# Kernel tuning notes

Hardware: AMD Instinct MI355X
Metric: run time of the kernel (lower is better)

Reference implementation:

```python
import jax, jax.numpy as jnp
import numpy as np

B, LAT, H, F, L, NL = 128, 128, 512, 128, 256, 2


def setup_inputs() -> dict:
    key = jax.random.key(0)
    ks = jax.random.split(key, 20)
    s = 0.05  # keep recurrence well-conditioned
    def n(k, shp):
        return jax.random.normal(k, shp, dtype=jnp.float32) * s
    return dict(
        z=jax.random.normal(ks[0], (B, LAT), dtype=jnp.float32),
        W_l2h=n(ks[1], (H * NL, LAT)), b_l2h=n(ks[2], (H * NL,)),
        W_l2c=n(ks[3], (H * NL, LAT)), b_l2c=n(ks[4], (H * NL,)),
        W_zp=n(ks[5], (H, LAT)), b_zp=n(ks[6], (H,)),
        W_ih0=n(ks[7], (4 * H, F + H)), W_hh0=n(ks[8], (4 * H, H)),
        b_ih0=n(ks[9], (4 * H,)), b_hh0=n(ks[10], (4 * H,)),
        W_ih1=n(ks[11], (4 * H, H)), W_hh1=n(ks[12], (4 * H, H)),
        b_ih1=n(ks[13], (4 * H,)), b_hh1=n(ks[14], (4 * H,)),
        ln_g=jnp.ones((H,), jnp.float32), ln_b=jnp.zeros((H,), jnp.float32),
        W_pre=n(ks[15], (H, H)), b_pre=n(ks[16], (H,)),
        W_out=n(ks[17], (F, H)), b_out=n(ks[18], (F,)),
    )


def _lstm_cell(x, h, c, Wih, Whh, bih, bhh):
    # PyTorch gate order: i, f, g, o
    gates = x @ Wih.T + bih + h @ Whh.T + bhh
    i, f, g, o = jnp.split(gates, 4, axis=-1)
    c = jax.nn.sigmoid(f) * c + jax.nn.sigmoid(i) * jnp.tanh(g)
    h = jax.nn.sigmoid(o) * jnp.tanh(c)
    return h, c


def _layernorm(x, g, b, eps=1e-5):
    m = jnp.mean(x, axis=-1, keepdims=True)
    v = jnp.var(x, axis=-1, keepdims=True)
    return (x - m) * jax.lax.rsqrt(v + eps) * g + b


def reference(z, W_l2h, b_l2h, W_l2c, b_l2c, W_zp, b_zp,
              W_ih0, W_hh0, b_ih0, b_hh0, W_ih1, W_hh1, b_ih1, b_hh1,
              ln_g, ln_b, W_pre, b_pre, W_out, b_out):
    # Faithful to torch: (B, NL*H) viewed row-major as (NL, B, H)
    h0 = (z @ W_l2h.T + b_l2h).reshape(NL, B, H)
    c0 = (z @ W_l2c.T + b_l2c).reshape(NL, B, H)
    z_proj = z @ W_zp.T + b_zp  # (B, H), injected every step
    dec0 = jnp.zeros((B, F), dtype=z.dtype)

    def step(carry, _):
        ha, ca, hb, cb, dec = carry
        x = jnp.concatenate([dec, z_proj], axis=-1)  # (B, F+H)
        ha, ca = _lstm_cell(x, ha, ca, W_ih0, W_hh0, b_ih0, b_hh0)
        hb, cb = _lstm_cell(ha, hb, cb, W_ih1, W_hh1, b_ih1, b_hh1)
        ln = _layernorm(hb, ln_g, ln_b)
        pre = jax.nn.relu(ln @ W_pre.T + b_pre)
        out_t = (pre + ln) @ W_out.T + b_out  # residual through MLP
        return (ha, ca, hb, cb, out_t), out_t

    _, ys = jax.lax.scan(step, (h0[0], c0[0], h0[1], c0[1], dec0), None, length=L)
    return jnp.transpose(ys, (1, 0, 2))  # (B, L, F)
```

## Files before the change

kernel.cpp:

```cpp
#include <hip/hip_runtime.h>
#include <hip/hip_cooperative_groups.h>

namespace cg = cooperative_groups;


typedef unsigned int uint32;
typedef unsigned short u16;
typedef __attribute__((ext_vector_type(8))) short bf16x8;
typedef __attribute__((ext_vector_type(4))) float f32x4;

static constexpr int Ln = 256, Fn = 128;
static constexpr int APS = 65536;
static constexpr int WPS = 2097152;
static constexpr int OPS = 65536;
static constexpr int PPS = 262144;

static constexpr int BAR_REL = 4096;
static constexpr int BAR_WORDS = 4160;

static constexpr int ROWP = 520;
static constexpr int PLANE = 16 * ROWP;
static constexpr int SACT_ELEMS = 6 * PLANE;

static constexpr int SM_HV   = 0;
static constexpr int SM_LNH  = 33024;
static constexpr int SM_LNM  = 49664;
static constexpr int SM_LNL  = 66304;
static constexpr int SM_RED  = 82944;
static constexpr int SM_MEAN = 83968;
static constexpr int SM_RSTD = 84032;
static constexpr int SMEM_BYTES = 84096;

__device__ __forceinline__ u16 f2bf(float f) {
  union { float f; uint32 u; } v; v.f = f;
  uint32 u = v.u + 0x7fffu + ((v.u >> 16) & 1u);
  return (u16)(u >> 16);
}
__device__ __forceinline__ float bf2f(u16 h) {
  union { uint32 u; float f; } v; v.u = ((uint32)h) << 16;
  return v.f;
}
__device__ __forceinline__ void splitbf3(float v, u16* hi, u16* mid, u16* lo) {
  u16 h = f2bf(v);
  float r = v - bf2f(h);
  u16 m = f2bf(r);
  float r2 = r - bf2f(m);
  *hi = h; *mid = m; *lo = f2bf(r2);
}
__device__ __forceinline__ float sigm(float x) { return 1.f / (1.f + expf(-x)); }
__device__ __forceinline__ bf16x8 ldf(const u16* p) { return *(const bf16x8*)p; }

__device__ __forceinline__ bf16x8 ldc16(const u16* p) {
  bf16x8 r;
  asm volatile("global_load_dwordx4 %0, %1, off sc0 sc1" : "=v"(r) : "v"(p) : "memory");
  return r;
}
__device__ __forceinline__ void stc2(u16* p, u16 v) {
  asm volatile("global_store_short %0, %1, off sc0 sc1" :: "v"(p), "v"((uint32)v) : "memory");
}
__device__ __forceinline__ void vwait0_fence() {
  asm volatile("s_waitcnt vmcnt(0)" ::: "memory");
  __builtin_amdgcn_sched_barrier(0);
}

__device__ __forceinline__ void gbar(uint32* arr, uint32* rel, uint32 ep, int blk) {
  asm volatile("s_waitcnt vmcnt(0) lgkmcnt(0)" ::: "memory");
  __syncthreads();
  int tid = threadIdx.x;
  if (blk == 0) {
    for (;;) {
      uint32 v = __hip_atomic_load(&arr[tid * 16], __ATOMIC_RELAXED, __HIP_MEMORY_SCOPE_AGENT);
      if (__syncthreads_and((tid == 0) || (v >= ep))) break;
      __builtin_amdgcn_s_sleep(1);
    }
    if (tid == 0)
      __hip_atomic_store(rel, ep, __ATOMIC_RELAXED, __HIP_MEMORY_SCOPE_AGENT);
  } else {
    if (tid == 0) {
      __hip_atomic_store(&arr[blk * 16], ep, __ATOMIC_RELAXED, __HIP_MEMORY_SCOPE_AGENT);
      while (__hip_atomic_load(rel, __ATOMIC_RELAXED, __HIP_MEMORY_SCOPE_AGENT) < ep)
        __builtin_amdgcn_s_sleep(1);
    }
  }
  __syncthreads();
  __builtin_amdgcn_sched_barrier(0);
}

#define MFMA1(A, B, ACC) ACC = __builtin_amdgcn_mfma_f32_16x16x32_bf16((A), (B), (ACC), 0, 0, 0)
#define MFMA6(AH, AM, AL, BH, BM, BL, A0, A1, A2) \
  do {                                            \
    MFMA1(AH, BH, A0);                            \
    MFMA1(AH, BM, A1); MFMA1(AM, BH, A1);         \
    MFMA1(AH, BL, A2); MFMA1(AL, BH, A2);         \
    MFMA1(AM, BM, A2);                            \
  } while (0)


__device__ __forceinline__ void stage_side(const u16* __restrict__ g, int b0,
                                           u16* sAct, int sideBase, int tid) {
  bf16x8 tv[12];
#pragma unroll
  for (int jr = 0; jr < 12; ++jr) {
    int plane = jr >> 2;
    int c2 = tid + ((jr & 3) << 8);
    int row = c2 >> 6, col = c2 & 63;
    tv[jr] = ldc16(g + (size_t)plane * APS + (size_t)(b0 + row) * 512 + col * 8);
  }
  vwait0_fence();
#pragma unroll
  for (int jr = 0; jr < 12; ++jr) {
    int plane = jr >> 2;
    int c2 = tid + ((jr & 3) << 8);
    int row = c2 >> 6, col = c2 & 63;
    *(bf16x8*)&sAct[sideBase + plane * PLANE + row * ROWP + col * 8] = tv[jr];
  }
}

__device__ __forceinline__ void gate_tile_p(
    const u16* __restrict__ g0, const u16* __restrict__ g1,
    const u16* __restrict__ wr,
    const float* __restrict__ bias, int bias_stride,
    float& cr, u16* __restrict__ hout,
    int b0, int h0, int tid, u16* sAct, float (*gbuf)[16][16]) {
  stage_side(g0, b0, sAct, 0, tid);
  stage_side(g1, b0, sAct, 3 * PLANE, tid);
  __syncthreads();
  int lane = tid & 63, w = tid >> 6, q = lane >> 4, r16 = lane & 15;
  const u16* aB = sAct + r16 * ROWP + q * 8;
  f32x4 A0 = {0.f, 0.f, 0.f, 0.f}, A1 = {0.f, 0.f, 0.f, 0.f}, A2 = {0.f, 0.f, 0.f, 0.f};
#pragma unroll
  for (int kb = 0; kb < 16; ++kb) {
    bf16x8 ah = ldf(aB + kb * 32), am = ldf(aB + PLANE + kb * 32), al = ldf(aB + 2 * PLANE + kb * 32);
    bf16x8 bh = ldf(wr + kb * 32), bm = ldf(wr + WPS + kb * 32), bl = ldf(wr + 2 * WPS + kb * 32);
    MFMA6(ah, am, al, bh, bm, bl, A0, A1, A2);
  }
#pragma unroll
  for (int kb = 0; kb < 16; ++kb) {
    bf16x8 ah = ldf(aB + 3 * PLANE + kb * 32), am = ldf(aB + 4 * PLANE + kb * 32),
           al = ldf(aB + 5 * PLANE + kb * 32);
    bf16x8 bh = ldf(wr + 512 + kb * 32), bm = ldf(wr + WPS + 512 + kb * 32),
           bl = ldf(wr + 2 * WPS + 512 + kb * 32);
    MFMA6(ah, am, al, bh, bm, bl, A0, A1, A2);
  }
#pragma unroll
  for (int r = 0; r < 4; ++r)
    gbuf[w][q * 4 + r][r16] = (A2[r] + A1[r]) + A0[r];
  __syncthreads();
  int bl_ = tid >> 4, hl = tid & 15;
  int b = b0 + bl_, h = h0 + hl;
  const float* bb = bias + (size_t)b * bias_stride;
  float gi = gbuf[0][bl_][hl] + bb[h];
  float gf = gbuf[1][bl_][hl] + bb[512 + h];
  float gc = gbuf[2][bl_][hl] + bb[1024 + h];
  float go = gbuf[3][bl_][hl] + bb[1536 + h];
  int idx = b * 512 + h;
  float cn = sigm(gf) * cr + sigm(gi) * tanhf(gc);
  cr = cn;
  float hv_ = sigm(go) * tanhf(cn);
  u16 hh, hm, hl2;
  splitbf3(hv_, &hh, &hm, &hl2);
  stc2(hout + idx, hh);
  stc2(hout + APS + idx, hm);
  stc2(hout + 2 * APS + idx, hl2);
}

__device__ __forceinline__ void ys_tile_p(
    const u16* __restrict__ sg, const u16* __restrict__ wr,
    const float* __restrict__ b_out, float* __restrict__ ys,
    int tout, int b0, int f0, int tid, u16* sAct) {
  stage_side(sg, b0, sAct, 0, tid);
  __syncthreads();
  int lane = tid & 63, q = lane >> 4, r16 = lane & 15;
  const u16* aB = sAct + r16 * ROWP + q * 8;
  f32x4 A0 = {0.f, 0.f, 0.f, 0.f}, A1 = {0.f, 0.f, 0.f, 0.f}, A2 = {0.f, 0.f, 0.f, 0.f};
#pragma unroll
  for (int kb = 0; kb < 16; ++kb) {
    bf16x8 ah = ldf(aB + kb * 32), am = ldf(aB + PLANE + kb * 32), al = ldf(aB + 2 * PLANE + kb * 32);
    bf16x8 bh = ldf(wr + kb * 32), bm = ldf(wr + OPS + kb * 32), bl = ldf(wr + 2 * OPS + kb * 32);
    MFMA6(ah, am, al, bh, bm, bl, A0, A1, A2);
  }
  int fc = f0 + r16;
  float bo = b_out[fc];
#pragma unroll
  for (int r = 0; r < 4; ++r) {
    int b = b0 + q * 4 + r;
    ys[(size_t)b * (Ln * Fn) + (size_t)tout * Fn + fc] = ((A2[r] + A1[r]) + A0[r]) + bo;
  }
}

__device__ __forceinline__ void lnpre_tile_p(
    const u16* __restrict__ hb, const u16* __restrict__ wr,
    const float* __restrict__ lng, const float* __restrict__ lnb,
    const float* __restrict__ b_pre, u16* __restrict__ s_out,
    int j0, int b0, int tid, char* smem) {
  float* hv = (float*)(smem + SM_HV);
  u16* lnH = (u16*)(smem + SM_LNH);
  u16* lnM = (u16*)(smem + SM_LNM);
  u16* lnL = (u16*)(smem + SM_LNL);
  float (*red)[16] = (float (*)[16])(smem + SM_RED);
  float* smean = (float*)(smem + SM_MEAN);
  float* srstd = (float*)(smem + SM_RSTD);
  bf16x8 p[12];
#pragma unroll
  for (int jj = 0; jj < 4; ++jj) {
    int c = tid + 256 * jj;
    int b = c >> 6, k0 = (c & 63) * 8;
    size_t base = (size_t)(b0 + b) * 512 + k0;
    p[jj * 3 + 0] = ldc16(hb + base);
    p[jj * 3 + 1] = ldc16(hb + APS + base);
    p[jj * 3 + 2] = ldc16(hb + 2 * APS + base);
  }
  vwait0_fence();
#pragma unroll
  for (int jj = 0; jj < 4; ++jj) {
    int c = tid + 256 * jj;
    int b = c >> 6, k0 = (c & 63) * 8;
#pragma unroll
    for (int e = 0; e < 8; ++e)
      hv[b * 516 + k0 + e] = (bf2f((u16)p[jj * 3 + 2][e]) + bf2f((u16)p[jj * 3 + 1][e])) +
                             bf2f((u16)p[jj * 3 + 0][e]);
  }
  __syncthreads();
  int bl_ = tid >> 4, kc = tid & 15;
  {
    float sm = 0.f;
    for (int kk = 0; kk < 32; ++kk) sm += hv[bl_ * 516 + kc * 32 + kk];
    red[bl_][kc] = sm;
  }
  __syncthreads();
  if (tid < 16) {
    float s1 = 0.f;
    for (int i = 0; i < 16; ++i) s1 += red[tid][i];
    smean[tid] = s1 * (1.f / 512.f);
  }
  __syncthreads();
  {
    float m = smean[bl_], sq = 0.f;
    for (int kk = 0; kk < 32; ++kk) {
      float d = hv[bl_ * 516 + kc * 32 + kk] - m;
      sq += d * d;
    }
    red[bl_][kc] = sq;
  }
  __syncthreads();
  if (tid < 16) {
    float s2 = 0.f;
    for (int i = 0; i < 16; ++i) s2 += red[tid][i];
    srstd[tid] = 1.f / sqrtf(s2 * (1.f / 512.f) + 1e-5f);
  }
  __syncthreads();
  for (int i = tid; i < 16 * 512; i += 256) {
    int b = i >> 9, k = i & 511;
    float v = (hv[b * 516 + k] - smean[b]) * srstd[b] * lng[k] + lnb[k];
    splitbf3(v, &lnH[b * 520 + k], &lnM[b * 520 + k], &lnL[b * 520 + k]);
  }
  __syncthreads();
  int lane = tid & 63, w = tid >> 6, q = lane >> 4, r16 = lane & 15;
  const u16* aH = lnH + r16 * 520 + q * 8;
  const u16* aM = lnM + r16 * 520 + q * 8;
  const u16* aL = lnL + r16 * 520 + q * 8;
  f32x4 A0 = {0.f, 0.f, 0.f, 0.f}, A1 = {0.f, 0.f, 0.f, 0.f}, A2 = {0.f, 0.f, 0.f, 0.f};
#pragma unroll
  for (int kb = 0; kb < 16; ++kb) {
    bf16x8 ah = ldf(aH + kb * 32), am = ldf(aM + kb * 32), al = ldf(aL + kb * 32);
    bf16x8 bh = ldf(wr + kb * 32), bm = ldf(wr + PPS + kb * 32), bl = ldf(wr + 2 * PPS + kb * 32);
    MFMA6(ah, am, al, bh, bm, bl, A0, A1, A2);
  }
  int j = j0 + w * 16 + r16;
  float bp = b_pre[j];
#pragma unroll
  for (int r = 0; r < 4; ++r) {
    int b = q * 4 + r;
    float lnv = (hv[b * 516 + j] - smean[b]) * srstd[b] * lng[j] + lnb[j];
    float pre = fmaxf(((A2[r] + A1[r]) + A0[r]) + bp, 0.f);
    float sval = pre + lnv;
    size_t sidx = (size_t)(b0 + b) * 512 + j;
    u16 sh, sm_, sl;
    splitbf3(sval, &sh, &sm_, &sl);
    stc2(s_out + sidx, sh);
    stc2(s_out + APS + sidx, sm_);
    stc2(s_out + 2 * APS + sidx, sl);
  }
}


__device__ __forceinline__ void gate_tile(
    const u16* __restrict__ a0, const u16* __restrict__ a1,
    const u16* __restrict__ wr,
    const float* __restrict__ bias, int bias_stride,
    float* __restrict__ cstate, u16* __restrict__ hout,
    int b0, int h0, int tid, float (*gbuf)[16][16]) {
  int w = tid >> 6;
  int lane = tid & 63, q = lane >> 4, r16 = lane & 15;
  f32x4 A0 = {0.f, 0.f, 0.f, 0.f}, A1 = {0.f, 0.f, 0.f, 0.f}, A2 = {0.f, 0.f, 0.f, 0.f};
#pragma unroll
  for (int kb = 0; kb < 16; ++kb) {
    bf16x8 ah = ldf(a0 + kb * 32), am = ldf(a0 + APS + kb * 32), al = ldf(a0 + 2 * APS + kb * 32);
    bf16x8 bh = ldf(wr + kb * 32), bm = ldf(wr + WPS + kb * 32), bl = ldf(wr + 2 * WPS + kb * 32);
    MFMA6(ah, am, al, bh, bm, bl, A0, A1, A2);
  }
#pragma unroll
  for (int kb = 0; kb < 16; ++kb) {
    bf16x8 ah = ldf(a1 + kb * 32), am = ldf(a1 + APS + kb * 32), al = ldf(a1 + 2 * APS + kb * 32);
    bf16x8 bh = ldf(wr + 512 + kb * 32), bm = ldf(wr + WPS + 512 + kb * 32),
           bl = ldf(wr + 2 * WPS + 512 + kb * 32);
    MFMA6(ah, am, al, bh, bm, bl, A0, A1, A2);
  }
#pragma unroll
  for (int r = 0; r < 4; ++r)
    gbuf[w][q * 4 + r][r16] = (A2[r] + A1[r]) + A0[r];
  __syncthreads();
  int bl_ = tid >> 4, hl = tid & 15;
  int b = b0 + bl_, h = h0 + hl;
  const float* bb = bias + (size_t)b * bias_stride;
  float gi = gbuf[0][bl_][hl] + bb[h];
  float gf = gbuf[1][bl_][hl] + bb[512 + h];
  float gc = gbuf[2][bl_][hl] + bb[1024 + h];
  float go = gbuf[3][bl_][hl] + bb[1536 + h];
  int idx = b * 512 + h;
  float c = cstate[idx];
  float cn = sigm(gf) * c + sigm(gi) * tanhf(gc);
  cstate[idx] = cn;
  float hv_ = sigm(go) * tanhf(cn);
  splitbf3(hv_, &hout[idx], &hout[APS + idx], &hout[2 * APS + idx]);
  __syncthreads();
}

__device__ __forceinline__ void ys_tile(
    const u16* __restrict__ a, const u16* __restrict__ wr,
    const float* __restrict__ b_out, float* __restrict__ ys,
    int tout, int b0, int f0, int tid) {
  int lane = tid & 63, q = lane >> 4, r16 = lane & 15;
  f32x4 A0 = {0.f, 0.f, 0.f, 0.f}, A1 = {0.f, 0.f, 0.f, 0.f}, A2 = {0.f, 0.f, 0.f, 0.f};
#pragma unroll
  for (int kb = 0; kb < 16; ++kb) {
    bf16x8 ah = ldf(a + kb * 32), am = ldf(a + APS + kb * 32), al = ldf(a + 2 * APS + kb * 32);
    bf16x8 bh = ldf(wr + kb * 32), bm = ldf(wr + OPS + kb * 32), bl = ldf(wr + 2 * OPS + kb * 32);
    MFMA6(ah, am, al, bh, bm, bl, A0, A1, A2);
  }
  int fc = f0 + r16;
  float bo = b_out[fc];
#pragma unroll
  for (int r = 0; r < 4; ++r) {
    int b = b0 + q * 4 + r;
    ys[(size_t)b * (Ln * Fn) + (size_t)tout * Fn + fc] = ((A2[r] + A1[r]) + A0[r]) + bo;
  }
}

__device__ __forceinline__ void lnpre_tile(
    const u16* __restrict__ hb, const u16* __restrict__ wr,
    const float* __restrict__ lng, const float* __restrict__ lnb,
    const float* __restrict__ b_pre, u16* __restrict__ s_out,
    int j0, int b0, int tid, char* smem) {
  float* hv = (float*)(smem + SM_HV);
  u16* lnH = (u16*)(smem + SM_LNH);
  u16* lnM = (u16*)(smem + SM_LNM);
  u16* lnL = (u16*)(smem + SM_LNL);
  float (*red)[16] = (float (*)[16])(smem + SM_RED);
  float* smean = (float*)(smem + SM_MEAN);
  float* srstd = (float*)(smem + SM_RSTD);
  for (int i = tid; i < 16 * 512; i += 256) {
    int b = i >> 9, k = i & 511;
    size_t hidx = (size_t)(b0 + b) * 512 + k;
    hv[b * 516 + k] = (bf2f(hb[2 * APS + hidx]) + bf2f(hb[APS + hidx])) + bf2f(hb[hidx]);
  }
  __syncthreads();
  int bl_ = tid >> 4, kc = tid & 15;
  {
    float sm = 0.f;
    for (int kk = 0; kk < 32; ++kk) sm += hv[bl_ * 516 + kc * 32 + kk];
    red[bl_][kc] = sm;
  }
  __syncthreads();
  if (tid < 16) {
    float s1 = 0.f;
    for (int i = 0; i < 16; ++i) s1 += red[tid][i];
    smean[tid] = s1 * (1.f / 512.f);
  }
  __syncthreads();
  {
    float m = smean[bl_], sq = 0.f;
    for (int kk = 0; kk < 32; ++kk) {
      float d = hv[bl_ * 516 + kc * 32 + kk] - m;
      sq += d * d;
    }
    red[bl_][kc] = sq;
  }
  __syncthreads();
  if (tid < 16) {
    float s2 = 0.f;
    for (int i = 0; i < 16; ++i) s2 += red[tid][i];
    srstd[tid] = 1.f / sqrtf(s2 * (1.f / 512.f) + 1e-5f);
  }
  __syncthreads();
  for (int i = tid; i < 16 * 512; i += 256) {
    int b = i >> 9, k = i & 511;
    float v = (hv[b * 516 + k] - smean[b]) * srstd[b] * lng[k] + lnb[k];
    splitbf3(v, &lnH[b * 520 + k], &lnM[b * 520 + k], &lnL[b * 520 + k]);
  }
  __syncthreads();
  int lane = tid & 63, w = tid >> 6, q = lane >> 4, r16 = lane & 15;
  const u16* aH = lnH + r16 * 520 + q * 8;
  const u16* aM = lnM + r16 * 520 + q * 8;
  const u16* aL = lnL + r16 * 520 + q * 8;
  f32x4 A0 = {0.f, 0.f, 0.f, 0.f}, A1 = {0.f, 0.f, 0.f, 0.f}, A2 = {0.f, 0.f, 0.f, 0.f};
#pragma unroll
  for (int kb = 0; kb < 16; ++kb) {
    bf16x8 ah = ldf(aH + kb * 32), am = ldf(aM + kb * 32), al = ldf(aL + kb * 32);
    bf16x8 bh = ldf(wr + kb * 32), bm = ldf(wr + PPS + kb * 32), bl = ldf(wr + 2 * PPS + kb * 32);
    MFMA6(ah, am, al, bh, bm, bl, A0, A1, A2);
  }
  int j = j0 + w * 16 + r16;
  float bp = b_pre[j];
#pragma unroll
  for (int r = 0; r < 4; ++r) {
    int b = q * 4 + r;
    float lnv = (hv[b * 516 + j] - smean[b]) * srstd[b] * lng[j] + lnb[j];
    float pre = fmaxf(((A2[r] + A1[r]) + A0[r]) + bp, 0.f);
    float sval = pre + lnv;
    size_t sidx = (size_t)(b0 + b) * 512 + j;
    splitbf3(sval, &s_out[sidx], &s_out[APS + sidx], &s_out[2 * APS + sidx]);
  }
  __syncthreads();
}


__global__ void prep_hc0(const float* __restrict__ z,
                         const float* __restrict__ W_l2h, const float* __restrict__ b_l2h,
                         const float* __restrict__ W_l2c, const float* __restrict__ b_l2c,
                         u16* __restrict__ ha0, u16* __restrict__ hb0,
                         float* __restrict__ ca, float* __restrict__ cb) {
  int idx = blockIdx.x * 256 + threadIdx.x;
  int b = idx & 127, j = idx >> 7;
  float ah = b_l2h[j], ac = b_l2c[j];
  for (int k = 0; k < 128; ++k) {
    float zv = z[b * 128 + k];
    ah += zv * W_l2h[j * 128 + k];
    ac += zv * W_l2c[j * 128 + k];
  }
  int flat = b * 1024 + j;
  if (flat < 65536) {
    splitbf3(ah, &ha0[flat], &ha0[APS + flat], &ha0[2 * APS + flat]);
    ca[flat] = ac;
  } else {
    flat -= 65536;
    splitbf3(ah, &hb0[flat], &hb0[APS + flat], &hb0[2 * APS + flat]);
    cb[flat] = ac;
  }
}

__global__ void prep_zp(const float* __restrict__ z, const float* __restrict__ W_zp,
                        const float* __restrict__ b_zp, float* __restrict__ zp) {
  int idx = blockIdx.x * 256 + threadIdx.x;
  int b = idx & 127, h = idx >> 7;
  float a = b_zp[h];
  for (int k = 0; k < 128; ++k) a += z[b * 128 + k] * W_zp[h * 128 + k];
  zp[b * 512 + h] = a;
}

__global__ void prep_gz(const float* __restrict__ zp, const float* __restrict__ W_ih0,
                        const float* __restrict__ b_ih0, const float* __restrict__ b_hh0,
                        const float* __restrict__ b_out,
                        float* __restrict__ GZ0, float* __restrict__ GZ1) {
  int idx = blockIdx.x * 256 + threadIdx.x;
  int b = idx & 127, g = idx >> 7;
  const float* wr = W_ih0 + (size_t)g * 640;
  float a = b_ih0[g] + b_hh0[g];
  for (int k = 0; k < 512; ++k) a += zp[b * 512 + k] * wr[128 + k];
  float co = 0.f;
  for (int f = 0; f < 128; ++f) co += b_out[f] * wr[f];
  GZ0[b * 2048 + g] = a;
  GZ1[b * 2048 + g] = a + co;
}

__global__ void prep_waf(const float* __restrict__ W_out, const float* __restrict__ W_ih0,
                         const float* __restrict__ W_hh0, u16* __restrict__ WAf) {
  int idx = blockIdx.x * 256 + threadIdx.x;
  int k = idx & 1023, g = idx >> 10;
  float v;
  if (k < 512) {
    v = 0.f;
    const float* wr = W_ih0 + (size_t)g * 640;
    for (int f = 0; f < 128; ++f) v += W_out[f * 512 + k] * wr[f];
  } else {
    v = W_hh0[(size_t)g * 512 + (k - 512)];
  }
  splitbf3(v, &WAf[idx], &WAf[WPS + idx], &WAf[2 * WPS + idx]);
}

__global__ void prep_wbf(const float* __restrict__ W_ih1, const float* __restrict__ W_hh1,
                         u16* __restrict__ WBf) {
  int idx = blockIdx.x * 256 + threadIdx.x;
  int k = idx & 1023, g = idx >> 10;
  float v = (k < 512) ? W_ih1[(size_t)g * 512 + k] : W_hh1[(size_t)g * 512 + (k - 512)];
  splitbf3(v, &WBf[idx], &WBf[WPS + idx], &WBf[2 * WPS + idx]);
}

__global__ void prep_misc(const float* __restrict__ W_pre, const float* __restrict__ W_out,
                          const float* __restrict__ b_ih1, const float* __restrict__ b_hh1,
                          u16* __restrict__ WPf, u16* __restrict__ WOf,
                          float* __restrict__ gb1, u16* __restrict__ s,
                          uint32* __restrict__ bar) {
  int idx = blockIdx.x * 256 + threadIdx.x;
  if (idx < 262144) { splitbf3(W_pre[idx], &WPf[idx], &WPf[PPS + idx], &WPf[2 * PPS + idx]); return; }
  idx -= 262144;
  if (idx < 65536) { splitbf3(W_out[idx], &WOf[idx], &WOf[OPS + idx], &WOf[2 * OPS + idx]); return; }
  idx -= 65536;
  if (idx < 2048) { gb1[idx] = b_ih1[idx] + b_hh1[idx]; return; }
  idx -= 2048;
  if (idx < 196608) { s[idx] = 0; return; }
  idx -= 196608;
  if (idx < BAR_WORDS) bar[idx] = 0;
}


__global__ __launch_bounds__(256, 1) void loop_k(
    const u16* __restrict__ WAf, const u16* __restrict__ WBf,
    const u16* __restrict__ WPf, const u16* __restrict__ WOf,
    const float* __restrict__ GZ0, const float* __restrict__ GZ1,
    const float* __restrict__ gb1,
    const float* __restrict__ ca, const float* __restrict__ cb,
    u16* __restrict__ ha0, u16* __restrict__ ha1,
    u16* __restrict__ hb0, u16* __restrict__ hb1,
    u16* __restrict__ s0, u16* __restrict__ s1,
    const float* __restrict__ lng, const float* __restrict__ lnb,
    const float* __restrict__ b_pre, const float* __restrict__ b_out,
    float* __restrict__ ys, uint32* __restrict__ bar) {
  __shared__ __align__(16) u16 sAct[SACT_ELEMS];
  __shared__ float gbuf[4][16][16];
  int tid = threadIdx.x;
  int lane = tid & 63, w = tid >> 6, q = lane >> 4, r16 = lane & 15;
  int blk = blockIdx.x;
  uint32* arr = bar;
  uint32* rel = bar + BAR_REL;

  int gg = blk & 31, bg = blk >> 5;
  int h0A = gg * 16, b0A = bg * 16;
  size_t wro = (size_t)(w * 512 + h0A + r16) * 1024 + q * 8;
  const u16* wrA = WAf + wro;
  const u16* wrB = WBf + wro;

  int jg = blk & 7, bgC = blk >> 3;
  int j0 = jg * 64, b0C = bgC * 16;
  const u16* wrP = WPf + (size_t)(j0 + w * 16 + r16) * 512 + q * 8;

  int ob = (blk - 64) & 15;
  int bgY = ob >> 1, fh = ob & 1;
  int b0Y = bgY * 16, f0 = fh * 64 + w * 16;
  const u16* wrO = WOf + (size_t)(f0 + r16) * 512 + q * 8;

  int cidx = (b0A + (tid >> 4)) * 512 + h0A + (tid & 15);
  float cA = ca[cidx], cB = cb[cidx];

  uint32 ep = 0;
  for (int t = 0; t < Ln; ++t) {
    u16* sPrev = (t & 1) ? s0 : s1;
    u16* sNext = (t & 1) ? s1 : s0;
    u16* haIn  = (t & 1) ? ha1 : ha0;
    u16* haOut = (t & 1) ? ha0 : ha1;
    u16* hbIn  = (t & 1) ? hb1 : hb0;
    u16* hbOut = (t & 1) ? hb0 : hb1;

    gate_tile_p(sPrev, haIn, wrA, t ? GZ1 : GZ0, 2048, cA, haOut, b0A, h0A, tid, sAct, gbuf);
    gbar(arr, rel, ++ep, blk);
    gate_tile_p(haOut, hbIn, wrB, gb1, 0, cB, hbOut, b0A, h0A, tid, sAct, gbuf);
    gbar(arr, rel, ++ep, blk);
    if (blk < 64) {
      lnpre_tile_p(hbOut, wrP, lng, lnb, b_pre, sNext, j0, b0C, tid, (char*)sAct);
    } else if (blk < 80 && t > 0) {
      ys_tile_p(sPrev, wrO, b_out, ys, t - 1, b0Y, f0, tid, sAct);
    }
    gbar(arr, rel, ++ep, blk);
  }
  if (blk >= 64 && blk < 80) {
    ys_tile_p(s1, wrO, b_out, ys, Ln - 1, b0Y, f0, tid, sAct);
  }
}


__global__ void cell_k(const u16* __restrict__ x0, const u16* __restrict__ x1,
                       const u16* __restrict__ Wf,
                       const float* __restrict__ bias, int bias_stride,
                       float* __restrict__ cstate, u16* __restrict__ hout,
                       int n_gate_blocks,
                       const u16* sv, const u16* __restrict__ WOf,
                       const float* __restrict__ b_out, float* __restrict__ ys, int t) {
  __shared__ float gbuf[4][16][16];
  int tid = threadIdx.x;
  int lane = tid & 63, w = tid >> 6, q = lane >> 4, r16 = lane & 15;
  int blk = blockIdx.x;
  if (blk < n_gate_blocks) {
    int gg = blk & 31, bg = blk >> 5;
    int h0 = gg * 16, b0 = bg * 16;
    const u16* wr = Wf + (size_t)(w * 512 + h0 + r16) * 1024 + q * 8;
    size_t aoff = (size_t)(b0 + r16) * 512 + q * 8;
    gate_tile(x0 + aoff, x1 + aoff, wr, bias, bias_stride, cstate, hout, b0, h0, tid, gbuf);
  } else {
    if (t < 1) return;
    int ob = blk - n_gate_blocks;
    int bg = ob >> 1, fh = ob & 1;
    int b0 = bg * 16, f0 = fh * 64 + w * 16;
    const u16* wr = WOf + (size_t)(f0 + r16) * 512 + q * 8;
    size_t aoff = (size_t)(b0 + r16) * 512 + q * 8;
    ys_tile(sv + aoff, wr, b_out, ys, t - 1, b0, f0, tid);
  }
}

__global__ void lnpre_k(const u16* __restrict__ hb, const u16* __restrict__ WPf,
                        const float* __restrict__ lng, const float* __restrict__ lnb,
                        const float* __restrict__ b_pre, u16* __restrict__ s_out) {
  __shared__ __align__(16) char smem[SMEM_BYTES];
  int tid = threadIdx.x;
  int lane = tid & 63, w = tid >> 6, q = lane >> 4, r16 = lane & 15;
  int jg = blockIdx.x & 7, bg = blockIdx.x >> 3;
  int j0 = jg * 64, b0 = bg * 16;
  const u16* wr = WPf + (size_t)(j0 + w * 16 + r16) * 512 + q * 8;
  lnpre_tile(hb, wr, lng, lnb, b_pre, s_out, j0, b0, tid, smem);
}


extern "C" void kernel_launch(void* const* d_in, const int* in_sizes, int n_in,
                              void* d_out, int out_size, void* d_ws, size_t ws_size,
                              hipStream_t stream) {
  const float* z     = (const float*)d_in[0];
  const float* W_l2h = (const float*)d_in[1];
  const float* b_l2h = (const float*)d_in[2];
  const float* W_l2c = (const float*)d_in[3];
  const float* b_l2c = (const float*)d_in[4];
  const float* W_zp  = (const float*)d_in[5];
  const float* b_zp  = (const float*)d_in[6];
  const float* W_ih0 = (const float*)d_in[7];
  const float* W_hh0 = (const float*)d_in[8];
  const float* b_ih0 = (const float*)d_in[9];
  const float* b_hh0 = (const float*)d_in[10];
  const float* W_ih1 = (const float*)d_in[11];
  const float* W_hh1 = (const float*)d_in[12];
  const float* b_ih1 = (const float*)d_in[13];
  const float* b_hh1 = (const float*)d_in[14];
  const float* ln_g  = (const float*)d_in[15];
  const float* ln_b  = (const float*)d_in[16];
  const float* W_pre = (const float*)d_in[17];
  const float* b_pre = (const float*)d_in[18];
  const float* W_out = (const float*)d_in[19];
  const float* b_out = (const float*)d_in[20];
  float* out = (float*)d_out;
  char* ws = (char*)d_ws;

  size_t off = 0;
  auto alloc = [&](size_t bytes) { void* p = ws + off; off += bytes; return p; };
  u16*   WAf  = (u16*)alloc(12582912);
  u16*   WBf  = (u16*)alloc(12582912);
  u16*   WPf  = (u16*)alloc(1572864);
  u16*   WOf  = (u16*)alloc(393216);
  float* GZ0  = (float*)alloc(1048576);
  float* GZ1  = (float*)alloc(1048576);
  float* gb1  = (float*)alloc(8192);
  float* zp   = (float*)alloc(262144);
  u16*   ha[2], *hbuf[2], *sb[2];
  ha[0]   = (u16*)alloc(393216);
  ha[1]   = (u16*)alloc(393216);
  hbuf[0] = (u16*)alloc(393216);
  hbuf[1] = (u16*)alloc(393216);
  float* ca   = (float*)alloc(262144);
  float* cb   = (float*)alloc(262144);
  sb[0]   = (u16*)alloc(393216);
  sb[1]   = (u16*)alloc(393216);
  uint32* bar = (uint32*)alloc(32768);

  prep_hc0<<<512, 256, 0, stream>>>(z, W_l2h, b_l2h, W_l2c, b_l2c, ha[0], hbuf[0], ca, cb);
  prep_zp<<<256, 256, 0, stream>>>(z, W_zp, b_zp, zp);
  prep_gz<<<1024, 256, 0, stream>>>(zp, W_ih0, b_ih0, b_hh0, b_out, GZ0, GZ1);
  prep_waf<<<8192, 256, 0, stream>>>(W_out, W_ih0, W_hh0, WAf);
  prep_wbf<<<8192, 256, 0, stream>>>(W_ih1, W_hh1, WBf);
  prep_misc<<<2073, 256, 0, stream>>>(W_pre, W_out, b_ih1, b_hh1, WPf, WOf, gb1, sb[1], bar);

  static int coop_supported = -1;
  if (coop_supported < 0) {
    int dev = 0;
    (void)hipGetDevice(&dev);
    int v = 0;
    (void)hipDeviceGetAttribute(&v, hipDeviceAttributeCooperativeLaunch, dev);
    coop_supported = v;
  }

  bool did_coop = false;
  if (coop_supported) {
    void* kargs[] = {
        (void*)&WAf, (void*)&WBf, (void*)&WPf, (void*)&WOf,
        (void*)&GZ0, (void*)&GZ1, (void*)&gb1, (void*)&ca, (void*)&cb,
        (void*)&ha[0], (void*)&ha[1], (void*)&hbuf[0], (void*)&hbuf[1],
        (void*)&sb[0], (void*)&sb[1],
        (void*)&ln_g, (void*)&ln_b, (void*)&b_pre, (void*)&b_out, (void*)&out,
        (void*)&bar};
    hipError_t err = hipLaunchCooperativeKernel((const void*)loop_k, dim3(256), dim3(256),
                                                kargs, 0, stream);
    did_coop = (err == hipSuccess);
  }

  if (!did_coop) {
    for (int t = 0; t < Ln; ++t) {
      u16* sPrev = (t & 1) ? sb[0] : sb[1];
      u16* sNext = (t & 1) ? sb[1] : sb[0];
      u16* haIn = ha[t & 1];
      u16* haOut = ha[(t + 1) & 1];
      u16* hbIn = hbuf[t & 1];
      u16* hbOut = hbuf[(t + 1) & 1];
      cell_k<<<272, 256, 0, stream>>>(sPrev, haIn, WAf, t ? GZ1 : GZ0, 2048,
                                      ca, haOut, 256, sPrev, WOf, b_out, out, t);
      cell_k<<<256, 256, 0, stream>>>(haOut, hbIn, WBf, gb1, 0,
                                      cb, hbOut, 256, sPrev, WOf, b_out, out, 0);
      lnpre_k<<<64, 256, 0, stream>>>(hbOut, WPf, ln_g, ln_b, b_pre, sNext);
    }
    cell_k<<<16, 256, 0, stream>>>(sb[1], ha[0], WAf, GZ1, 2048, ca, ha[1],
                                   0, sb[1], WOf, b_out, out, Ln);
  }
}
```

Measured before the change: 14.31 ms.

## Replace global grid barrier with per-batch-group barriers of 32 blocks

Blocks are regrouped so that each batch group of 16 rows (32 blocks sharing blk>>5) owns its whole pipeline: gates, LN/pre projection (gg<8) and output projection (gg 8-9) for its own batch rows. Since batch rows are independent, the central grid barrier with a master block is replaced by a decentralized barrier in which each block waits only on the 32 blocks of its group. This is meant to cut barrier latency and remove the serialization through block 0, at the cost of all 32 flags being polled by every block and a work remapping that must match the tile functions' batch indexing.

```diff
diff --git a/kernel.cpp b/kernel.cpp
--- a/kernel.cpp
+++ b/kernel.cpp
@@ -15,8 +15,7 @@
 static constexpr int OPS = 65536;
 static constexpr int PPS = 262144;
 
-static constexpr int BAR_REL = 4096;
-static constexpr int BAR_WORDS = 4160;
+static constexpr int BAR_WORDS = 4096;
 
 static constexpr int ROWP = 520;
 static constexpr int PLANE = 16 * ROWP;
@@ -63,26 +62,20 @@
   __builtin_amdgcn_sched_barrier(0);
 }
 
-__device__ __forceinline__ void gbar(uint32* arr, uint32* rel, uint32 ep, int blk) {
+__device__ __forceinline__ void gbar_g(uint32* arr, uint32 ep, int blk) {
   asm volatile("s_waitcnt vmcnt(0) lgkmcnt(0)" ::: "memory");
   __syncthreads();
   int tid = threadIdx.x;
-  if (blk == 0) {
-    for (;;) {
-      uint32 v = __hip_atomic_load(&arr[tid * 16], __ATOMIC_RELAXED, __HIP_MEMORY_SCOPE_AGENT);
-      if (__syncthreads_and((tid == 0) || (v >= ep))) break;
-      __builtin_amdgcn_s_sleep(1);
-    }
-    if (tid == 0)
-      __hip_atomic_store(rel, ep, __ATOMIC_RELAXED, __HIP_MEMORY_SCOPE_AGENT);
-  } else {
-    if (tid == 0) {
-      __hip_atomic_store(&arr[blk * 16], ep, __ATOMIC_RELAXED, __HIP_MEMORY_SCOPE_AGENT);
-      while (__hip_atomic_load(rel, __ATOMIC_RELAXED, __HIP_MEMORY_SCOPE_AGENT) < ep)
-        __builtin_amdgcn_s_sleep(1);
-    }
-  }
-  __syncthreads();
+  if (tid == 0)
+    __hip_atomic_store(&arr[blk * 16], ep, __ATOMIC_RELAXED, __HIP_MEMORY_SCOPE_AGENT);
+  int base = (blk >> 5) << 5;
+  for (;;) {
+    uint32 v = (tid < 32)
+        ? __hip_atomic_load(&arr[(base + tid) * 16], __ATOMIC_RELAXED, __HIP_MEMORY_SCOPE_AGENT)
+        : ep;
+    if (__syncthreads_and(v >= ep)) break;
+    __builtin_amdgcn_s_sleep(1);
+  }
   __builtin_amdgcn_sched_barrier(0);
 }
 
@@ -531,8 +524,6 @@
   int tid = threadIdx.x;
   int lane = tid & 63, w = tid >> 6, q = lane >> 4, r16 = lane & 15;
   int blk = blockIdx.x;
-  uint32* arr = bar;
-  uint32* rel = bar + BAR_REL;
 
   int gg = blk & 31, bg = blk >> 5;
   int h0A = gg * 16, b0A = bg * 16;
@@ -540,13 +531,10 @@
   const u16* wrA = WAf + wro;
   const u16* wrB = WBf + wro;
 
-  int jg = blk & 7, bgC = blk >> 3;
-  int j0 = jg * 64, b0C = bgC * 16;
+  int j0 = gg * 64;
   const u16* wrP = WPf + (size_t)(j0 + w * 16 + r16) * 512 + q * 8;
-
-  int ob = (blk - 64) & 15;
-  int bgY = ob >> 1, fh = ob & 1;
-  int b0Y = bgY * 16, f0 = fh * 64 + w * 16;
+  int fh = gg & 1;
+  int f0 = fh * 64 + w * 16;
   const u16* wrO = WOf + (size_t)(f0 + r16) * 512 + q * 8;
 
   int cidx = (b0A + (tid >> 4)) * 512 + h0A + (tid & 15);
@@ -562,18 +550,18 @@
     u16* hbOut = (t & 1) ? hb0 : hb1;
 
     gate_tile_p(sPrev, haIn, wrA, t ? GZ1 : GZ0, 2048, cA, haOut, b0A, h0A, tid, sAct, gbuf);
-    gbar(arr, rel, ++ep, blk);
+    gbar_g(bar, ++ep, blk);
     gate_tile_p(haOut, hbIn, wrB, gb1, 0, cB, hbOut, b0A, h0A, tid, sAct, gbuf);
-    gbar(arr, rel, ++ep, blk);
-    if (blk < 64) {
-      lnpre_tile_p(hbOut, wrP, lng, lnb, b_pre, sNext, j0, b0C, tid, (char*)sAct);
-    } else if (blk < 80 && t > 0) {
-      ys_tile_p(sPrev, wrO, b_out, ys, t - 1, b0Y, f0, tid, sAct);
+    gbar_g(bar, ++ep, blk);
+    if (gg < 8) {
+      lnpre_tile_p(hbOut, wrP, lng, lnb, b_pre, sNext, j0, b0A, tid, (char*)sAct);
+    } else if (gg < 10 && t > 0) {
+      ys_tile_p(sPrev, wrO, b_out, ys, t - 1, b0A, f0, tid, sAct);
     }
-    gbar(arr, rel, ++ep, blk);
-  }
-  if (blk >= 64 && blk < 80) {
-    ys_tile_p(s1, wrO, b_out, ys, Ln - 1, b0Y, f0, tid, sAct);
+    gbar_g(bar, ++ep, blk);
+  }
+  if (gg >= 8 && gg < 10) {
+    ys_tile_p(s1, wrO, b_out, ys, Ln - 1, b0A, f0, tid, sAct);
   }
 }
 
```

Result: slower. 14.95 ms (+4.5%).
